# Kernel tuning notes

Hardware: AMD Instinct MI355X
Metric: run time of the kernel (lower is better)

Reference implementation:

```python
import jax, jax.numpy as jnp
import numpy as np

K = 20
BN_SCALE = 1.0 / np.sqrt(1.0 + 1e-5)  # BN at init: running_mean=0, running_var=1


def _graph_feature(x, k):
    # x: (B, N, C) point features -> (B, N, k, 2C) edge features
    sq = jnp.sum(x * x, axis=-1)  # (B, N)
    # negative squared distance: larger == closer (matches torch topk on -dist)
    d = 2.0 * jnp.einsum('bnc,bmc->bnm', x, x) - sq[:, :, None] - sq[:, None, :]
    idx = jax.lax.top_k(d, k)[1]  # (B, N, k), self included as nearest
    nbr = jax.vmap(lambda pts, i: pts[i])(x, idx)  # (B, N, k, C) gather
    ctr = jnp.broadcast_to(x[:, :, None, :], nbr.shape)
    return jnp.concatenate([nbr - ctr, ctr], axis=-1)


def _edge_conv(e, W, g, b):
    # 1x1 Conv2d (no bias) + BatchNorm(init stats) + LeakyReLU(0.2) + max over k
    y = jnp.einsum('bnkc,oc->bnko', e, W)
    y = jax.nn.leaky_relu(y * (g * BN_SCALE) + b, 0.2)
    return jnp.max(y, axis=2)  # (B, N, O)


def setup_inputs() -> dict:
    key = jax.random.key(0)
    ks = jax.random.split(key, 12)
    B, N = 4, 1024
    dims_in = [6, 128, 256, 512]
    dims_out = [64, 128, 256, 512]
    inp = {'x': jax.random.normal(ks[0], (B, N, 3), dtype=jnp.float32)}
    for i, (ci, co) in enumerate(zip(dims_in, dims_out), start=1):
        inp[f'W{i}'] = jax.random.normal(ks[i], (co, ci), dtype=jnp.float32) * (1.0 / np.sqrt(ci))
        inp[f'g{i}'] = jnp.ones((co,), dtype=jnp.float32)
        inp[f'b{i}'] = jnp.zeros((co,), dtype=jnp.float32)
    inp['W5'] = jax.random.normal(ks[5], (512, 960), dtype=jnp.float32) * (1.0 / np.sqrt(960.0))
    inp['g5'] = jnp.ones((512,), dtype=jnp.float32)
    inp['b5'] = jnp.zeros((512,), dtype=jnp.float32)
    inp['We'] = jax.random.normal(ks[6], (256, 512), dtype=jnp.float32) * (1.0 / np.sqrt(512.0))
    return inp


def reference(x, W1, g1, b1, W2, g2, b2, W3, g3, b3, W4, g4, b4, W5, g5, b5, We):
    x1 = _edge_conv(_graph_feature(x, K), W1, g1, b1)   # (B, N, 64)
    x2 = _edge_conv(_graph_feature(x1, K), W2, g2, b2)  # (B, N, 128)
    x3 = _edge_conv(_graph_feature(x2, K), W3, g3, b3)  # (B, N, 256)
    x4 = _edge_conv(_graph_feature(x3, K), W4, g4, b4)  # (B, N, 512)
    xc = jnp.concatenate([x1, x2, x3, x4], axis=-1)     # (B, N, 960)
    y = jnp.einsum('bnc,oc->bno', xc, W5)               # conv5 (1x1 Conv1d)
    y = jax.nn.leaky_relu(y * (g5 * BN_SCALE) + b5, 0.2)
    feat = jnp.max(y, axis=1)                           # (B, 512) global max-pool
    return feat @ We.T                                  # (B, num_features)
```

## Files before the change

### kernel.cpp

```cpp
#include <hip/hip_runtime.h>
#include <hip/hip_bf16.h>
#include <math.h>

typedef __hip_bfloat16 bf16;
typedef __bf16 v8bf __attribute__((ext_vector_type(8)));
typedef float v4f __attribute__((ext_vector_type(4)));

#define BN_SCALE 0.9999950000374997f
#define NPTS 1024
#define NB 4
#define CH5 ((size_t)4 * 1024 * 512)

__device__ __forceinline__ float b2f(bf16 v) { return __bfloat162float(v); }
__device__ __forceinline__ bf16 f2b(float v) { return __float2bfloat16(v); }
__device__ __forceinline__ float ldw(const void* p, size_t i, int isf) {
    return isf ? ((const float*)p)[i] : b2f(((const bf16*)p)[i]);
}
__device__ __forceinline__ unsigned ordf(float f) {
    unsigned u = __float_as_uint(f);
    return (u & 0x80000000u) ? ~u : (u | 0x80000000u);
}
__device__ __forceinline__ float iordf(unsigned u) {
    return (u & 0x80000000u) ? __uint_as_float(u ^ 0x80000000u) : __uint_as_float(~u);
}

__device__ __forceinline__ int detect_isf(const void* xraw, int* cnt) {
    const unsigned short* u = (const unsigned short*)xraw;
    int t = threadIdx.x, c = 0;
    for (int i = t; i < 512; i += 256) {
        unsigned short v = u[i];
        int e = (v >> 7) & 0xFF;
        int m = v & 0x7F;
        if (e == 0xFF || e >= 141 || (e == 0 && m != 0)) c++;
    }
    cnt[t] = c;
    __syncthreads();
    for (int off = 128; off > 0; off >>= 1) {
        if (t < off) cnt[t] += cnt[t + off];
        __syncthreads();
    }
    int isf = (cnt[0] > 30) ? 1 : 0;
    __syncthreads();
    return isf;
}

__global__ void k_prep(const void* __restrict__ W1, const void* __restrict__ W2,
                       const void* __restrict__ W3, const void* __restrict__ W4,
                       const void* __restrict__ W5, const void* __restrict__ x,
                       bf16* __restrict__ Whi, bf16* __restrict__ Wlo,
                       bf16* __restrict__ xph, bf16* __restrict__ xpl, float* __restrict__ sq,
                       int* __restrict__ flag, unsigned* __restrict__ pooledU) {
    __shared__ int cnt[256];
    int isf = detect_isf(x, cnt);
    if (blockIdx.x == 0) {
        if (threadIdx.x == 0) *flag = isf;
        for (int i = threadIdx.x; i < 2048; i += 256) pooledU[i] = 0u;
    }
    int idx = blockIdx.x * 256 + threadIdx.x;
    if (idx < 839680) {
        const void* src; int C, O, two, r, c;
        if (idx < 4096)        { src = W1; C = 3;   O = 64;  two = 1; int lo = idx;          r = lo >> 5; c = lo & 31; }
        else if (idx < 20480)  { src = W2; C = 64;  O = 128; two = 1; int lo = idx - 4096;   r = lo >> 6; c = lo & 63; }
        else if (idx < 86016)  { src = W3; C = 128; O = 256; two = 1; int lo = idx - 20480;  r = lo >> 7; c = lo & 127; }
        else if (idx < 348160) { src = W4; C = 256; O = 512; two = 1; int lo = idx - 86016;  r = lo >> 8; c = lo & 255; }
        else                   { src = W5; C = 960; O = 512; two = 0; int lo = idx - 348160; r = lo / 960; c = lo - r * 960; }
        float wv = 0.f;
        if (c < C) {
            size_t off;
            if (two) off = (r < O) ? (size_t)r * 2 * C + c : (size_t)(r - O) * 2 * C + C + c;
            else     off = (size_t)r * C + c;
            wv = ldw(src, off, isf);
        }
        bf16 h = f2b(wv);
        Whi[idx] = h;
        Wlo[idx] = f2b(wv - b2f(h));
    } else if (idx < 843776) {
        int p = idx - 839680;
        int z = p >> 10, n = p & 1023;
        bf16* ph = xph + (size_t)z * NPTS * 32;
        bf16* pl = xpl + (size_t)z * NPTS * 32;
        float s = 0.f;
        for (int c = 0; c < 32; c++) {
            float v = (c < 3) ? ldw(x, (size_t)z * NPTS * 3 + n * 3 + c, isf) : 0.f;
            bf16 h = f2b(v);
            ph[n * 32 + c] = h;
            pl[n * 32 + c] = f2b(v - b2f(h));
            s += v * v;
        }
        sq[z * NPTS + n] = s;
    }
}

__device__ __forceinline__ int lidx(int plane, int row) {
    return ((((plane << 7) | row)) ^ (plane << 1)) << 3;
}
struct St2 { float4 a, b; };
__device__ __forceinline__ St2 ldStage(const bf16* src, int ld) {
    int t = threadIdx.x; int r = t >> 2, kq = t & 3;
    St2 s;
    s.a = *(const float4*)(src + (size_t)r * ld + kq * 8);
    s.b = *(const float4*)(src + (size_t)(r + 64) * ld + kq * 8);
    return s;
}
__device__ __forceinline__ void stStage(bf16* dst, const St2& s) {
    int t = threadIdx.x; int r = t >> 2, kq = t & 3;
    *(float4*)(dst + lidx(kq, r)) = s.a;
    *(float4*)(dst + lidx(kq, r + 64)) = s.b;
}
__device__ __forceinline__ void fill128(bf16* dst, const bf16* src, int ld) {
    int t = threadIdx.x;
    int r = t >> 2, kq = t & 3;
    *(float4*)(dst + lidx(kq, r))      = *(const float4*)(src + (size_t)r * ld + kq * 8);
    *(float4*)(dst + lidx(kq, r + 64)) = *(const float4*)(src + (size_t)(r + 64) * ld + kq * 8);
}
__device__ __forceinline__ v8bf ldf(const bf16* tile, int sub, int l) {
    return *(const v8bf*)(tile + lidx(l >> 4, sub * 16 + (l & 15)));
}

#define TSTRIDE 129

__global__ __launch_bounds__(256) void k_layer_a(const bf16* __restrict__ Xhi, const bf16* __restrict__ Xlo,
                                                 int ld, int Kpad, size_t xstride,
                                                 const bf16* __restrict__ Whi, const bf16* __restrict__ Wlo,
                                                 int O, const float* __restrict__ sqg,
                                                 float* __restrict__ Dg, float* __restrict__ Pg,
                                                 const int* __restrict__ flag) {
    int i = blockIdx.x;
    int z = (i >> 1) & 3;
    int bi = ((i >> 3) << 1) | (i & 1);
    const bf16* Xh = Xhi + (size_t)z * xstride;
    const bf16* Xl = Xlo + (size_t)z * xstride;
    __shared__ alignas(16) char smem[128 * TSTRIDE * 4];
    bf16* Ah = (bf16*)smem;
    bf16* Al = (bf16*)(smem + 16384);
    bf16* Bh = (bf16*)(smem + 32768);
    bf16* Bl = (bf16*)(smem + 49152);
    int w = threadIdx.x >> 6, l = threadIdx.x & 63;
    int wr = w >> 1, wc = w & 1;
    int quad = l >> 4, col = l & 15;
    v4f zero = {0.f, 0.f, 0.f, 0.f};
    v4f acc[4][4] = {{zero, zero, zero, zero}, {zero, zero, zero, zero},
                     {zero, zero, zero, zero}, {zero, zero, zero, zero}};

    if (bi < 36) {
        int bx = 0;
        while ((((bx + 1) * (bx + 2)) >> 1) <= bi) bx++;
        int by = bi - ((bx * (bx + 1)) >> 1);
        const float* sq = sqg + z * NPTS;
        float* D = Dg + (size_t)z * NPTS * NPTS;
        int n0 = by * 128, m0 = bx * 128;
        const bf16* pAn = Xh + (size_t)n0 * ld;
        const bf16* pAm = Xh + (size_t)m0 * ld;
        const bf16* pLn = Xl + (size_t)n0 * ld;
        const bf16* pLm = Xl + (size_t)m0 * ld;
        St2 sA = ldStage(pAn, ld), sB = ldStage(pAm, ld);
        St2 sC = ldStage(pLn, ld), sD = ldStage(pLm, ld);
        stStage(Ah, sA); stStage(Bh, sB);
        stStage(Al, sC); stStage(Bl, sD);
        __syncthreads();
        int cur = 0;
        for (int k0 = 0; k0 < Kpad; k0 += 32) {
            bool more = (k0 + 32 < Kpad);
            if (more) {
                sA = ldStage(pAn + k0 + 32, ld);
                sB = ldStage(pAm + k0 + 32, ld);
                sC = ldStage(pLn + k0 + 32, ld);
                sD = ldStage(pLm + k0 + 32, ld);
            }
            v8bf ah[4], al[4];
#pragma unroll
            for (int mi = 0; mi < 4; mi++) {
                ah[mi] = ldf(Ah + cur * 4096, wr * 4 + mi, l);
                al[mi] = ldf(Al + cur * 4096, wr * 4 + mi, l);
            }
#pragma unroll
            for (int ni = 0; ni < 4; ni++) {
                v8bf bh = ldf(Bh + cur * 4096, wc * 4 + ni, l);
                v8bf bl = ldf(Bl + cur * 4096, wc * 4 + ni, l);
#pragma unroll
                for (int mi = 0; mi < 4; mi++) {
                    acc[mi][ni] = __builtin_amdgcn_mfma_f32_16x16x32_bf16(ah[mi], bh, acc[mi][ni], 0, 0, 0);
                    acc[mi][ni] = __builtin_amdgcn_mfma_f32_16x16x32_bf16(ah[mi], bl, acc[mi][ni], 0, 0, 0);
                    acc[mi][ni] = __builtin_amdgcn_mfma_f32_16x16x32_bf16(al[mi], bh, acc[mi][ni], 0, 0, 0);
                }
            }
            if (more) {
                stStage(Ah + (cur ^ 1) * 4096, sA); stStage(Bh + (cur ^ 1) * 4096, sB);
                stStage(Al + (cur ^ 1) * 4096, sC); stStage(Bl + (cur ^ 1) * 4096, sD);
            }
            __syncthreads();
            cur ^= 1;
        }
        int rb = n0 + wr * 64 + quad * 4;
        int cb = m0 + wc * 64 + col;
        int rloc = wr * 64 + quad * 4;
        int cloc = wc * 64 + col;
        float* Tt = (float*)smem;
        float sm[4];
#pragma unroll
        for (int ni = 0; ni < 4; ni++) sm[ni] = sq[cb + ni * 16];
#pragma unroll
        for (int mi = 0; mi < 4; mi++) {
#pragma unroll
            for (int r = 0; r < 4; r++) {
                int row = rb + mi * 16 + r;
                float sn = sq[row];
#pragma unroll
                for (int ni = 0; ni < 4; ni++) {
                    float d = 2.f * acc[mi][ni][r] - sn - sm[ni];
                    D[(size_t)row * NPTS + cb + ni * 16] = d;
                    if (bx != by)
                        Tt[(cloc + ni * 16) * TSTRIDE + rloc + mi * 16 + r] = d;
                }
            }
        }
        if (bx != by) {
            __syncthreads();
            int t = threadIdx.x;
            int rl = t & 127, ch = t >> 7;
            float* Dm = D + (size_t)m0 * NPTS + n0;
#pragma unroll 4
            for (int it = 0; it < 64; it++) {
                int cl = it * 2 + ch;
                Dm[(size_t)cl * NPTS + rl] = Tt[cl * TSTRIDE + rl];
            }
        }
    } else {
        int isf = *flag;
        int nCol = (2 * O) >> 7;
        int s = bi - 36;
        int n0 = (s % nCol) * 128;
        int m0 = (s / nCol) * 128;
        int N2 = 2 * O;
        float* P = Pg + (size_t)z * NPTS * N2;
        const bf16* pXh = Xh + (size_t)m0 * ld;
        const bf16* pXl = Xl + (size_t)m0 * ld;
        const bf16* pWh = Whi + (size_t)n0 * Kpad;
        const bf16* pWl = Wlo + (size_t)n0 * Kpad;
        St2 sA = ldStage(pXh, ld), sC = ldStage(pXl, ld);
        St2 sB = ldStage(pWh, Kpad), sD;
        if (isf) sD = ldStage(pWl, Kpad);
        stStage(Ah, sA); stStage(Al, sC); stStage(Bh, sB);
        if (isf) stStage(Bl, sD);
        __syncthreads();
        int cur = 0;
        for (int k0 = 0; k0 < Kpad; k0 += 32) {
            bool more = (k0 + 32 < Kpad);
            if (more) {
                sA = ldStage(pXh + k0 + 32, ld);
                sC = ldStage(pXl + k0 + 32, ld);
                sB = ldStage(pWh + k0 + 32, Kpad);
                if (isf) sD = ldStage(pWl + k0 + 32, Kpad);
            }
            v8bf ah[4], al[4];
#pragma unroll
            for (int mi = 0; mi < 4; mi++) {
                ah[mi] = ldf(Ah + cur * 4096, wr * 4 + mi, l);
                al[mi] = ldf(Al + cur * 4096, wr * 4 + mi, l);
            }
#pragma unroll
            for (int ni = 0; ni < 4; ni++) {
                v8bf bh = ldf(Bh + cur * 4096, wc * 4 + ni, l);
#pragma unroll
                for (int mi = 0; mi < 4; mi++) {
                    acc[mi][ni] = __builtin_amdgcn_mfma_f32_16x16x32_bf16(ah[mi], bh, acc[mi][ni], 0, 0, 0);
                    acc[mi][ni] = __builtin_amdgcn_mfma_f32_16x16x32_bf16(al[mi], bh, acc[mi][ni], 0, 0, 0);
                }
                if (isf) {
                    v8bf bl = ldf(Bl + cur * 4096, wc * 4 + ni, l);
#pragma unroll
                    for (int mi = 0; mi < 4; mi++)
                        acc[mi][ni] = __builtin_amdgcn_mfma_f32_16x16x32_bf16(ah[mi], bl, acc[mi][ni], 0, 0, 0);
                }
            }
            if (more) {
                stStage(Ah + (cur ^ 1) * 4096, sA); stStage(Al + (cur ^ 1) * 4096, sC);
                stStage(Bh + (cur ^ 1) * 4096, sB);
                if (isf) stStage(Bl + (cur ^ 1) * 4096, sD);
            }
            __syncthreads();
            cur ^= 1;
        }
        int rb = m0 + wr * 64 + quad * 4;
        int cb = n0 + wc * 64 + col;
#pragma unroll
        for (int mi = 0; mi < 4; mi++)
#pragma unroll
            for (int r = 0; r < 4; r++) {
                int row = rb + mi * 16 + r;
#pragma unroll
                for (int ni = 0; ni < 4; ni++)
                    P[(size_t)row * N2 + cb + ni * 16] = acc[mi][ni][r];
            }
    }
}

template<int CTRL>
__device__ __forceinline__ void dpp_fmax(float& bv) {
    int ov = __builtin_amdgcn_update_dpp(__float_as_int(bv), __float_as_int(bv), CTRL, 0xF, 0xF, false);
    bv = fmaxf(bv, __int_as_float(ov));
}
template<int CTRL>
__device__ __forceinline__ void dpp_umin(unsigned& m) {
    unsigned om = (unsigned)__builtin_amdgcn_update_dpp((int)m, (int)m, CTRL, 0xF, 0xF, false);
    m = m < om ? m : om;
}
#define PICK(va, ja, vb, jb, vo, jo) { bool t_ = (vb) > (va); vo = t_ ? (vb) : (va); jo = t_ ? (jb) : (ja); }

__device__ __forceinline__ float max20(const float* v) {
    float a0 = fmaxf(fmaxf(v[0], v[1]), v[2]);
    float a1 = fmaxf(fmaxf(v[3], v[4]), v[5]);
    float a2 = fmaxf(fmaxf(v[6], v[7]), v[8]);
    float a3 = fmaxf(fmaxf(v[9], v[10]), v[11]);
    float a4 = fmaxf(fmaxf(v[12], v[13]), v[14]);
    float a5 = fmaxf(fmaxf(v[15], v[16]), v[17]);
    float a6 = fmaxf(v[18], v[19]);
    float b0 = fmaxf(fmaxf(a0, a1), a2);
    float b1 = fmaxf(fmaxf(a3, a4), a5);
    return fmaxf(fmaxf(b0, b1), a6);
}
__device__ __forceinline__ float min20(const float* v) {
    float a0 = fminf(fminf(v[0], v[1]), v[2]);
    float a1 = fminf(fminf(v[3], v[4]), v[5]);
    float a2 = fminf(fminf(v[6], v[7]), v[8]);
    float a3 = fminf(fminf(v[9], v[10]), v[11]);
    float a4 = fminf(fminf(v[12], v[13]), v[14]);
    float a5 = fminf(fminf(v[15], v[16]), v[17]);
    float a6 = fminf(v[18], v[19]);
    float b0 = fminf(fminf(a0, a1), a2);
    float b1 = fminf(fminf(a3, a4), a5);
    return fminf(fminf(b0, b1), a6);
}

__global__ __launch_bounds__(256) void k_layer_b(const float* __restrict__ Dg, const float* __restrict__ Pg,
                                                 const void* __restrict__ g, const void* __restrict__ bias,
                                                 int O, bf16* __restrict__ xhOut, bf16* __restrict__ xlOut,
                                                 float* __restrict__ sqOut, int writeSq,
                                                 const int* __restrict__ flag) {
    __shared__ int ids[4][20];
    int isf = *flag;
    int i = blockIdx.x;
    int z = (i >> 1) & 3;
    int local = ((i >> 3) << 1) | (i & 1);
    int tid = threadIdx.x;
    int wq = tid >> 6, l = tid & 63;
    int row = local * 4 + wq;

    {
        const float* Dr = Dg + (size_t)z * NPTS * NPTS + (size_t)row * NPTS;
        float v[16];
#pragma unroll
        for (int jj = 0; jj < 4; jj++) {
            float4 f4 = *(const float4*)(Dr + jj * 256 + l * 4);
            v[jj * 4 + 0] = f4.x; v[jj * 4 + 1] = f4.y;
            v[jj * 4 + 2] = f4.z; v[jj * 4 + 3] = f4.w;
        }
        float bmv[4]; int bmj[4];
#pragma unroll
        for (int gg = 0; gg < 4; gg++) {
            float a0, a1; int j0, j1;
            PICK(v[4 * gg + 0], 4 * gg + 0, v[4 * gg + 1], 4 * gg + 1, a0, j0);
            PICK(v[4 * gg + 2], 4 * gg + 2, v[4 * gg + 3], 4 * gg + 3, a1, j1);
            PICK(a0, j0, a1, j1, bmv[gg], bmj[gg]);
        }
        float candv; int candj, candi;
        {
            float t0, t1; int s0, s1;
            PICK(bmv[0], bmj[0], bmv[1], bmj[1], t0, s0);
            PICK(bmv[2], bmj[2], bmv[3], bmj[3], t1, s1);
            PICK(t0, s0, t1, s1, candv, candj);
            candi = (candj >> 2) * 256 + l * 4 + (candj & 3);
        }
        for (int s = 0; s < 20; s++) {
            float bv = candv;
            dpp_fmax<0xB1>(bv);
            dpp_fmax<0x4E>(bv);
            dpp_fmax<0x124>(bv);
            dpp_fmax<0x128>(bv);
            dpp_fmax<0x142>(bv);
            dpp_fmax<0x143>(bv);
            float gmax = __int_as_float(__builtin_amdgcn_readlane(__float_as_int(bv), 63));
            unsigned long long mask = __ballot(candv == gmax);
            int bii;
            if (__popcll(mask) == 1) {
                int srcl = __ffsll((unsigned long long)mask) - 1;
                bii = __builtin_amdgcn_readlane(candi, srcl);
            } else {
                unsigned mi = (candv == gmax) ? (unsigned)candi : 0xFFFFFFFFu;
                dpp_umin<0xB1>(mi);
                dpp_umin<0x4E>(mi);
                dpp_umin<0x124>(mi);
                dpp_umin<0x128>(mi);
                dpp_umin<0x142>(mi);
                dpp_umin<0x143>(mi);
                bii = __builtin_amdgcn_readlane((int)mi, 63);
            }
            if (l == 0) ids[wq][s] = bii;
            if (candi == bii) {
                int ej = (bii >> 8) * 4 + (bii & 3);
                int eg = ej >> 2, ek = ej & 3;
#pragma unroll
                for (int gg = 0; gg < 4; gg++) if (gg == eg) {
#pragma unroll
                    for (int kk = 0; kk < 4; kk++)
                        if (kk == ek) v[4 * gg + kk] = -__builtin_inff();
                    float a0, a1; int j0, j1;
                    PICK(v[4 * gg + 0], 4 * gg + 0, v[4 * gg + 1], 4 * gg + 1, a0, j0);
                    PICK(v[4 * gg + 2], 4 * gg + 2, v[4 * gg + 3], 4 * gg + 3, a1, j1);
                    PICK(a0, j0, a1, j1, bmv[gg], bmj[gg]);
                }
                float t0, t1; int s0, s1;
                PICK(bmv[0], bmj[0], bmv[1], bmj[1], t0, s0);
                PICK(bmv[2], bmj[2], bmv[3], bmj[3], t1, s1);
                PICK(t0, s0, t1, s1, candv, candj);
                candi = (candj >> 2) * 256 + l * 4 + (candj & 3);
            }
        }
    }

    int N2 = 2 * O;
    const float* P = Pg + (size_t)z * NPTS * N2;
    int offj[20];
#pragma unroll
    for (int j = 0; j < 20; j++)
        offj[j] = __builtin_amdgcn_readfirstlane(ids[wq][j]) * N2;
    int n = row;
    const float* Pn = P + (size_t)n * N2;
    float tot = 0.f;
    int nc = O >> 6;
    for (int c = 0; c < nc; c++) {
        int o = c * 64 + l;
        float scl = ldw(g, o, isf) * BN_SCALE;
        float bb = ldw(bias, o, isf);
        float tv = Pn[O + o] - Pn[o];
        float vv[20];
#pragma unroll
        for (int j = 0; j < 20; j++) vv[j] = P[offj[j] + o];
        float mx = max20(vv);
        float base;
        if (__ballot(scl < 0.f) != 0) {
            float mn = min20(vv);
            base = (scl >= 0.f ? mx : mn) + tv;
        } else {
            base = mx + tv;
        }
        float accv = base * scl + bb;
        accv = accv > 0.f ? accv : 0.2f * accv;
        bf16 hi = f2b(accv);
        bf16 lo = f2b(accv - b2f(hi));
        xhOut[(size_t)z * NPTS * 960 + (size_t)n * 960 + o] = hi;
        xlOut[(size_t)z * NPTS * 960 + (size_t)n * 960 + o] = lo;
        if (writeSq) {
            float xv = b2f(hi) + b2f(lo);
            float s2 = xv * xv;
#pragma unroll
            for (int off = 32; off > 0; off >>= 1) s2 += __shfl_down(s2, off);
            if (l == 0) tot += s2;
        }
    }
    if (writeSq && l == 0) sqOut[z * NPTS + row] = tot;
}

__global__ __launch_bounds__(256) void k_conv5(const bf16* __restrict__ Xhi, const bf16* __restrict__ Xlo,
                                               const bf16* __restrict__ Whi, const bf16* __restrict__ Wlo,
                                               float* __restrict__ P5,
                                               const int* __restrict__ flag) {
    int isf = *flag;
    int i = blockIdx.x;
    int z = (i >> 1) & 3;
    int rest = ((i >> 3) << 1) | (i & 1);
    int ks = rest >> 5;
    int tile = rest & 31;
    int m0 = (tile >> 2) * 128, o0 = (tile & 3) * 128;
    const bf16* Xh = Xhi + (size_t)z * NPTS * 960;
    const bf16* Xl = Xlo + (size_t)z * NPTS * 960;
    __shared__ alignas(16) bf16 Ah[4096], Al[4096], Bh[4096], Bl[4096];
    int w = threadIdx.x >> 6, l = threadIdx.x & 63;
    int wr = w >> 1, wc = w & 1;
    int quad = l >> 4, col = l & 15;
    v4f zero = {0.f, 0.f, 0.f, 0.f};
    v4f acc[4][4] = {{zero, zero, zero, zero}, {zero, zero, zero, zero},
                     {zero, zero, zero, zero}, {zero, zero, zero, zero}};
    int kbeg = ks * 160, kend = kbeg + 160;
    for (int k0 = kbeg; k0 < kend; k0 += 32) {
        __syncthreads();
        fill128(Ah, Xh + (size_t)m0 * 960 + k0, 960);
        fill128(Al, Xl + (size_t)m0 * 960 + k0, 960);
        fill128(Bh, Whi + (size_t)o0 * 960 + k0, 960);
        if (isf) fill128(Bl, Wlo + (size_t)o0 * 960 + k0, 960);
        __syncthreads();
        v8bf ah[4], al[4];
#pragma unroll
        for (int mi = 0; mi < 4; mi++) {
            ah[mi] = ldf(Ah, wr * 4 + mi, l);
            al[mi] = ldf(Al, wr * 4 + mi, l);
        }
#pragma unroll
        for (int ni = 0; ni < 4; ni++) {
            v8bf bh = ldf(Bh, wc * 4 + ni, l);
#pragma unroll
            for (int mi = 0; mi < 4; mi++) {
                acc[mi][ni] = __builtin_amdgcn_mfma_f32_16x16x32_bf16(ah[mi], bh, acc[mi][ni], 0, 0, 0);
                acc[mi][ni] = __builtin_amdgcn_mfma_f32_16x16x32_bf16(al[mi], bh, acc[mi][ni], 0, 0, 0);
            }
            if (isf) {
                v8bf bl = ldf(Bl, wc * 4 + ni, l);
#pragma unroll
                for (int mi = 0; mi < 4; mi++)
                    acc[mi][ni] = __builtin_amdgcn_mfma_f32_16x16x32_bf16(ah[mi], bl, acc[mi][ni], 0, 0, 0);
            }
        }
    }
    float* Pw = P5 + (size_t)ks * CH5 + (size_t)z * NPTS * 512;
    int rb = m0 + wr * 64 + quad * 4;
    int cb = o0 + wc * 64 + col;
#pragma unroll
    for (int mi = 0; mi < 4; mi++)
#pragma unroll
        for (int r = 0; r < 4; r++) {
            int row = rb + mi * 16 + r;
#pragma unroll
            for (int ni = 0; ni < 4; ni++)
                Pw[(size_t)row * 512 + cb + ni * 16] = acc[mi][ni][r];
        }
}

__global__ __launch_bounds__(256) void k_pool5(const float* __restrict__ P5,
                                               const void* __restrict__ g, const void* __restrict__ bias,
                                               unsigned* __restrict__ pooledU,
                                               const int* __restrict__ flag) {
    __shared__ float red2[128];
    int isf = *flag;
    int i = blockIdx.x;
    int z = (i >> 1) & 3;
    int rest = ((i >> 3) << 1) | (i & 1);
    int oc = (rest & 3) * 128, mc = (rest >> 2) * 32;
    int t = threadIdx.x;
    int c = t & 127, h = t >> 7;
    int o = oc + c;
    float scl = ldw(g, o, isf) * BN_SCALE;
    float bb = ldw(bias, o, isf);
    const float* p0 = P5 + (size_t)z * NPTS * 512 + (size_t)(mc + h * 16) * 512 + o;
    float ym = -__builtin_inff();
    for (int r = 0; r < 16; r++) {
        const float* p = p0 + (size_t)r * 512;
        float s = p[0];
#pragma unroll
        for (int ks = 1; ks < 6; ks++) s += p[(size_t)ks * CH5];
        float v = s * scl + bb;
        v = v > 0.f ? v : 0.2f * v;
        ym = fmaxf(ym, v);
    }
    if (h == 1) red2[c] = ym;
    __syncthreads();
    if (h == 0) {
        float m = fmaxf(ym, red2[c]);
        atomicMax(&pooledU[z * 512 + o], ordf(m));
    }
}

__global__ void k_final(const unsigned* __restrict__ pooledU, const void* __restrict__ We,
                        void* __restrict__ out, const int* __restrict__ flag) {
    __shared__ float p[512];
    int isf = *flag;
    int b = blockIdx.x >> 2, fb = blockIdx.x & 3;
    int t = threadIdx.x, w = t >> 6, l = t & 63;
    for (int i = t; i < 512; i += 256) p[i] = iordf(pooledU[b * 512 + i]);
    __syncthreads();
    for (int it = 0; it < 16; it++) {
        int f = fb * 64 + w * 16 + it;
        float s = 0.f;
        size_t base = (size_t)f * 512 + l * 8;
#pragma unroll
        for (int j = 0; j < 8; j++) s += p[l * 8 + j] * ldw(We, base + j, isf);
#pragma unroll
        for (int off = 32; off > 0; off >>= 1) s += __shfl_down(s, off);
        if (l == 0) {
            if (isf) ((float*)out)[b * 256 + f] = s;
            else     ((bf16*)out)[b * 256 + f] = f2b(s);
        }
    }
}

extern "C" void kernel_launch(void* const* d_in, const int* in_sizes, int n_in,
                              void* d_out, int out_size, void* d_ws, size_t ws_size,
                              hipStream_t stream) {
    const void* x  = d_in[0];
    const void* Wl[4] = { d_in[1], d_in[4], d_in[7], d_in[10] };
    const void* gl[4] = { d_in[2], d_in[5], d_in[8], d_in[11] };
    const void* bl[4] = { d_in[3], d_in[6], d_in[9], d_in[12] };
    const void* W5 = d_in[13];
    const void* g5 = d_in[14];
    const void* b5 = d_in[15];
    const void* We = d_in[16];

    char* base = (char*)d_ws;
    bf16*     xc_hi   = (bf16*)(base);
    bf16*     xc_lo   = (bf16*)(base + 7864320);
    bf16*     xpadh   = (bf16*)(base + 15728640);
    bf16*     xpadl   = (bf16*)(base + 15990784);
    float*    Dbuf    = (float*)(base + 16252928);
    float*    Pbuf    = (float*)(base + 33030144);
    bf16*     Whi     = (bf16*)(base + 49807360);
    bf16*     Wlo     = (bf16*)(base + 51486720);
    unsigned* pooledU = (unsigned*)(base + 53493760);
    float*    sq      = (float*)(base + 53501952);
    int*      flag    = (int*)(base + 53518336);
    float*    P5      = (float*)(base + 53520384);

    const int Kpad[4]   = { 32, 64, 128, 256 };
    const int Os[4]     = { 64, 128, 256, 512 };
    const int Woff[5]   = { 0, 4096, 20480, 86016, 348160 };
    const int colIn[4]  = { 0, 0, 64, 192 };
    const int colOut[4] = { 0, 64, 192, 448 };

    k_prep<<<3296, 256, 0, stream>>>(Wl[0], Wl[1], Wl[2], Wl[3], W5, x,
                                     Whi, Wlo, xpadh, xpadl, sq, flag, pooledU);

    for (int l = 0; l < 4; l++) {
        int O = Os[l];
        int nCol = (2 * O) >> 7;
        int nBlk = 36 + 8 * nCol;
        const bf16* Xh = (l == 0) ? xpadh : (xc_hi + colIn[l]);
        const bf16* Xl = (l == 0) ? xpadl : (xc_lo + colIn[l]);
        int ld = (l == 0) ? 32 : 960;
        size_t xstr = (l == 0) ? (size_t)NPTS * 32 : (size_t)NPTS * 960;
        k_layer_a<<<nBlk * NB, 256, 0, stream>>>(
            Xh, Xl, ld, Kpad[l], xstr, Whi + Woff[l], Wlo + Woff[l], O, sq, Dbuf, Pbuf, flag);
        k_layer_b<<<NPTS * NB / 4, 256, 0, stream>>>(
            Dbuf, Pbuf, gl[l], bl[l], O, xc_hi + colOut[l], xc_lo + colOut[l], sq, l < 3, flag);
    }
    k_conv5<<<768, 256, 0, stream>>>(xc_hi, xc_lo, Whi + Woff[4], Wlo + Woff[4], P5, flag);
    k_pool5<<<512, 256, 0, stream>>>(P5, g5, b5, pooledU, flag);
    k_final<<<16, 256, 0, stream>>>(pooledU, We, d_out, flag);
}
```

Measured before the change: 276.7 us.

## Overlap weight split-conversion for later layers with layer-1 distance kernel

The prep kernel now converts only W1 and the padded input points. The bf16 hi/lo split of W2..W5 moves into extra blocks appended to the layer-1 k_layer_a grid. Those blocks exit early after converting weights, so the conversion runs alongside the small layer-1 GEMM instead of serialising ahead of it. The cost is a larger layer-1 grid and a branch at the top of k_layer_a.

Measured after the change: 274.5 us. No clear change (-0.8%).

```diff
diff --git a/kernel.cpp b/kernel.cpp
--- a/kernel.cpp
+++ b/kernel.cpp
@@ -44,12 +44,10 @@
     return isf;
 }
 
-__global__ void k_prep(const void* __restrict__ W1, const void* __restrict__ W2,
-                       const void* __restrict__ W3, const void* __restrict__ W4,
-                       const void* __restrict__ W5, const void* __restrict__ x,
-                       bf16* __restrict__ Whi, bf16* __restrict__ Wlo,
-                       bf16* __restrict__ xph, bf16* __restrict__ xpl, float* __restrict__ sq,
-                       int* __restrict__ flag, unsigned* __restrict__ pooledU) {
+__global__ void k_prep1(const void* __restrict__ W1, const void* __restrict__ x,
+                        bf16* __restrict__ Whi, bf16* __restrict__ Wlo,
+                        bf16* __restrict__ xph, bf16* __restrict__ xpl, float* __restrict__ sq,
+                        int* __restrict__ flag, unsigned* __restrict__ pooledU) {
     __shared__ int cnt[256];
     int isf = detect_isf(x, cnt);
     if (blockIdx.x == 0) {
@@ -57,25 +55,18 @@
         for (int i = threadIdx.x; i < 2048; i += 256) pooledU[i] = 0u;
     }
     int idx = blockIdx.x * 256 + threadIdx.x;
-    if (idx < 839680) {
-        const void* src; int C, O, two, r, c;
-        if (idx < 4096)        { src = W1; C = 3;   O = 64;  two = 1; int lo = idx;          r = lo >> 5; c = lo & 31; }
-        else if (idx < 20480)  { src = W2; C = 64;  O = 128; two = 1; int lo = idx - 4096;   r = lo >> 6; c = lo & 63; }
-        else if (idx < 86016)  { src = W3; C = 128; O = 256; two = 1; int lo = idx - 20480;  r = lo >> 7; c = lo & 127; }
-        else if (idx < 348160) { src = W4; C = 256; O = 512; two = 1; int lo = idx - 86016;  r = lo >> 8; c = lo & 255; }
-        else                   { src = W5; C = 960; O = 512; two = 0; int lo = idx - 348160; r = lo / 960; c = lo - r * 960; }
+    if (idx < 4096) {
+        int r = idx >> 5, c = idx & 31;
         float wv = 0.f;
-        if (c < C) {
-            size_t off;
-            if (two) off = (r < O) ? (size_t)r * 2 * C + c : (size_t)(r - O) * 2 * C + C + c;
-            else     off = (size_t)r * C + c;
-            wv = ldw(src, off, isf);
+        if (c < 3) {
+            size_t off = (r < 64) ? (size_t)r * 6 + c : (size_t)(r - 64) * 6 + 3 + c;
+            wv = ldw(W1, off, isf);
         }
         bf16 h = f2b(wv);
         Whi[idx] = h;
         Wlo[idx] = f2b(wv - b2f(h));
-    } else if (idx < 843776) {
-        int p = idx - 839680;
+    } else if (idx < 8192) {
+        int p = idx - 4096;
         int z = p >> 10, n = p & 1023;
         bf16* ph = xph + (size_t)z * NPTS * 32;
         bf16* pl = xpl + (size_t)z * NPTS * 32;
@@ -124,7 +115,30 @@
                                                  const bf16* __restrict__ Whi, const bf16* __restrict__ Wlo,
                                                  int O, const float* __restrict__ sqg,
                                                  float* __restrict__ Dg, float* __restrict__ Pg,
-                                                 const int* __restrict__ flag) {
+                                                 const int* __restrict__ flag, int tileBlocks,
+                                                 const void* __restrict__ W2, const void* __restrict__ W3,
+                                                 const void* __restrict__ W4, const void* __restrict__ W5,
+                                                 bf16* __restrict__ WhiAll, bf16* __restrict__ WloAll) {
+    if (blockIdx.x >= tileBlocks) {
+        int isf = *flag;
+        int idx = (blockIdx.x - tileBlocks) * 256 + threadIdx.x + 4096;
+        const void* src; int C, Ow, two, r, c;
+        if (idx < 20480)       { src = W2; C = 64;  Ow = 128; two = 1; int lo = idx - 4096;   r = lo >> 6; c = lo & 63; }
+        else if (idx < 86016)  { src = W3; C = 128; Ow = 256; two = 1; int lo = idx - 20480;  r = lo >> 7; c = lo & 127; }
+        else if (idx < 348160) { src = W4; C = 256; Ow = 512; two = 1; int lo = idx - 86016;  r = lo >> 8; c = lo & 255; }
+        else                   { src = W5; C = 960; Ow = 512; two = 0; int lo = idx - 348160; r = lo / 960; c = lo - r * 960; }
+        float wv = 0.f;
+        if (c < C) {
+            size_t off;
+            if (two) off = (r < Ow) ? (size_t)r * 2 * C + c : (size_t)(r - Ow) * 2 * C + C + c;
+            else     off = (size_t)r * C + c;
+            wv = ldw(src, off, isf);
+        }
+        bf16 h = f2b(wv);
+        WhiAll[idx] = h;
+        WloAll[idx] = f2b(wv - b2f(h));
+        return;
+    }
     int i = blockIdx.x;
     int z = (i >> 1) & 3;
     int bi = ((i >> 3) << 1) | (i & 1);
@@ -614,8 +628,7 @@
     const int colIn[4]  = { 0, 0, 64, 192 };
     const int colOut[4] = { 0, 64, 192, 448 };
 
-    k_prep<<<3296, 256, 0, stream>>>(Wl[0], Wl[1], Wl[2], Wl[3], W5, x,
-                                     Whi, Wlo, xpadh, xpadl, sq, flag, pooledU);
+    k_prep1<<<32, 256, 0, stream>>>(Wl[0], x, Whi, Wlo, xpadh, xpadl, sq, flag, pooledU);
 
     for (int l = 0; l < 4; l++) {
         int O = Os[l];
@@ -625,8 +638,11 @@
         const bf16* Xl = (l == 0) ? xpadl : (xc_lo + colIn[l]);
         int ld = (l == 0) ? 32 : 960;
         size_t xstr = (l == 0) ? (size_t)NPTS * 32 : (size_t)NPTS * 960;
-        k_layer_a<<<nBlk * NB, 256, 0, stream>>>(
-            Xh, Xl, ld, Kpad[l], xstr, Whi + Woff[l], Wlo + Woff[l], O, sq, Dbuf, Pbuf, flag);
+        int tileBlocks = nBlk * NB;
+        int grid = (l == 0) ? tileBlocks + 3264 : tileBlocks;
+        k_layer_a<<<grid, 256, 0, stream>>>(
+            Xh, Xl, ld, Kpad[l], xstr, Whi + Woff[l], Wlo + Woff[l], O, sq, Dbuf, Pbuf, flag,
+            tileBlocks, Wl[1], Wl[2], Wl[3], W5, Whi, Wlo);
         k_layer_b<<<NPTS * NB / 4, 256, 0, stream>>>(
             Dbuf, Pbuf, gl[l], bl[l], O, xc_hi + colOut[l], xc_lo + colOut[l], sq, l < 3, flag);
     }
```
